# Kernel tuning notes

Measured on AMD Instinct MI355X. Metric: run time of the kernel, lower is better.

## Reference

```python
import jax, jax.numpy as jnp
import numpy as np

# --- hashgrid config (from __init__: num_levels=16, level_dim=4, base_res=2, log2_hashmap_size=19, desired_res=2048) ---
NUM_LEVELS = 16
LEVEL_DIM = 4
BASE_RES = 2
DESIRED_RES = 2048
TABLE_SIZE = 2 ** 19
_b = np.exp((np.log(DESIRED_RES) - np.log(BASE_RES)) / (NUM_LEVELS - 1))
SCALES = BASE_RES * _b ** np.arange(NUM_LEVELS) - 1.0          # instant-ngp per-level scale
RES = (np.ceil(SCALES) + 1).astype(np.int64)                   # per-level grid resolution
PRIME = np.uint32(2654435761)                                  # 2D spatial hash prime


def softplus10(x):
    return jax.nn.softplus(10.0 * x) / 10.0


def hash_encode(u, tables):
    """u: [P,2] in [0,1]; tables: [L, TABLE_SIZE, LEVEL_DIM]. Returns [P, L*LEVEL_DIM]."""
    outs = []
    for l in range(NUM_LEVELS):
        s = float(SCALES[l])
        res = int(RES[l])
        pos = u * s + 0.5
        pf = jnp.floor(pos)
        fr = pos - pf                      # bilinear fractions, [P,2]
        pi = pf.astype(jnp.int32)
        acc = None
        for dx in (0, 1):
            for dy in (0, 1):
                cx = pi[:, 0] + dx
                cy = pi[:, 1] + dy
                if res * res <= TABLE_SIZE:
                    idx = cy * res + cx                                   # dense level
                else:
                    idx = (cx.astype(jnp.uint32) ^ (cy.astype(jnp.uint32) * PRIME)) % jnp.uint32(TABLE_SIZE)
                    idx = idx.astype(jnp.int32)                           # hashed level
                wx = fr[:, 0] if dx else 1.0 - fr[:, 0]
                wy = fr[:, 1] if dy else 1.0 - fr[:, 1]
                term = tables[l][idx] * (wx * wy)[:, None]                # gather + bilerp
                acc = term if acc is None else acc + term
        outs.append(acc)
    return jnp.concatenate(outs, axis=-1)


def setup_inputs() -> dict:
    key = jax.random.key(0)
    ks = jax.random.split(key, 4)
    B, N, T = 4, 2048, 192
    x = jax.random.normal(ks[0], (B, N, T, 2), jnp.float32)
    embeddings = jax.random.normal(ks[1], (NUM_LEVELS, TABLE_SIZE, LEVEL_DIM), jnp.float32) * 1e-2
    W0 = jax.random.normal(ks[2], (64, 64), jnp.float32) / 8.0
    b0 = jnp.zeros((64,), jnp.float32)
    W1 = jax.random.normal(ks[3], (64, 1), jnp.float32) / 8.0
    b1 = jnp.zeros((1,), jnp.float32)
    return {"x": x, "embeddings": embeddings, "W0": W0, "b0": b0, "W1": W1, "b1": b1}


def reference(x, embeddings, W0, b0, W1, b1):
    B, N, T = x.shape[:3]
    xf = x.reshape(-1, T, 2)                       # [B*N, T, 2]
    rays_o = xf[:, 0]
    rd = xf[:, -1] - xf[:, 0]
    rd = rd / jnp.linalg.norm(rd, axis=-1, keepdims=True)
    z = jnp.linspace(0.0, 2.0, T)                  # [T]
    sample_dist = 1.0 / T
    xys = rays_o[:, None, :] + rd[:, None, :] * z[None, :, None]   # [B*N, T, 2]
    xys = jnp.clip(xys, -1.0, 1.0)                 # aabb clamp [-1,-1,1,1]
    u = (xys.reshape(-1, 2) + 1.0) * 0.5           # map [-bound,bound] -> [0,1], bound=1
    feats = hash_encode(u, embeddings)             # [P, 64]
    h = softplus10(feats @ W0 + b0)
    sigma = softplus10(h @ W1 + b1).reshape(-1, T) # [B*N, T]
    deltas = jnp.concatenate([jnp.full((1,), sample_dist, sigma.dtype), z[1:] - z[:-1]])  # [T]
    density = (deltas[None, :] * sigma).reshape(B, N, T)
    return density
```

## Files before the change

kernel.cpp:

```cpp
#include <hip/hip_runtime.h>
#include <cmath>

#define NUM_LEVELS 16
#define TABLE_SIZE 524288
#define TMASK (TABLE_SIZE - 1)
#define HASH_PRIME 2654435761u
#define T_SAMPLES 192
#define BLOCK 256
#define PTS 64

typedef __bf16 bf16x8 __attribute__((ext_vector_type(8)));
typedef __bf16 bf16x4 __attribute__((ext_vector_type(4)));
typedef float f32x4 __attribute__((ext_vector_type(4)));

struct LvlParams {
    float s[NUM_LEVELS];
    int   res[NUM_LEVELS];
    int   hashed[NUM_LEVELS];
};

__device__ __forceinline__ float softplus10(float x) {
    float t = 10.0f * x;
    float e = __expf(-fabsf(t));
    return (fmaxf(t, 0.0f) + __logf(1.0f + e)) * 0.1f;
}

typedef __attribute__((address_space(1))) const void CGV;
typedef __attribute__((address_space(3))) void LDSV;

__device__ __forceinline__ void dma_gather16(const void* gaddr, void* lds_wave_base) {
    __builtin_amdgcn_global_load_lds((CGV*)gaddr, (LDSV*)lds_wave_base, 16, 0, 0);
}

__device__ __forceinline__ void corner_idx(int cx, int cy, int res, int hashed,
                                           int& i00, int& i01, int& i10, int& i11) {
    if (hashed) {
        unsigned hy0 = (unsigned)cy * HASH_PRIME;
        unsigned hy1 = (unsigned)(cy + 1) * HASH_PRIME;
        i00 = (int)(((unsigned)cx ^ hy0) & TMASK);
        i01 = (int)(((unsigned)cx ^ hy1) & TMASK);
        i10 = (int)(((unsigned)(cx + 1) ^ hy0) & TMASK);
        i11 = (int)(((unsigned)(cx + 1) ^ hy1) & TMASK);
    } else {
        i00 = cy * res + cx; i10 = i00 + 1;
        i01 = i00 + res;     i11 = i01 + 1;
    }
}

__device__ __forceinline__ bf16x4 lerp4(f32x4 c00, f32x4 c01, f32x4 c10, f32x4 c11,
                                        float fx, float fy) {
    float w00 = (1.0f - fx) * (1.0f - fy), w01 = (1.0f - fx) * fy;
    float w10 = fx * (1.0f - fy),          w11 = fx * fy;
    f32x4 a = c00 * w00 + c01 * w01 + c10 * w10 + c11 * w11;
    bf16x4 r;
    r[0] = (__bf16)a.x; r[1] = (__bf16)a.y; r[2] = (__bf16)a.z; r[3] = (__bf16)a.w;
    return r;
}

__global__ void prep(const float* __restrict__ W0, __bf16* __restrict__ w0f,
                     float* __restrict__ sArr, int* __restrict__ resArr,
                     int* __restrict__ hashArr, LvlParams lp) {
    const int t = threadIdx.x;
    if (t < NUM_LEVELS) {
        sArr[t] = lp.s[t]; resArr[t] = lp.res[t]; hashArr[t] = lp.hashed[t];
    }
    #pragma unroll
    for (int i = 0; i < 16; ++i) {
        int f = t * 16 + i;
        int j = f & 7, lx = (f >> 3) & 15, q = (f >> 7) & 3, nt = (f >> 9) & 3, kc = f >> 11;
        int k = kc * 32 + q * 8 + j;
        int n = nt * 16 + lx;
        w0f[f] = (__bf16)W0[k * 64 + n];
    }
}

__launch_bounds__(BLOCK, 5)
__global__ void nerf_fused(const float* __restrict__ x,
                           const float* __restrict__ emb,
                           const __bf16* __restrict__ w0f,
                           const float* __restrict__ sArr,
                           const int* __restrict__ resArr,
                           const int* __restrict__ hashArr,
                           const float* __restrict__ b0,
                           const float* __restrict__ W1,
                           const float* __restrict__ b1,
                           float* __restrict__ out) {
    __shared__ __align__(16) f32x4 land[16 * 64];
    __shared__ __align__(16) __bf16 feS[PTS][72];

    const int tid  = threadIdx.x;
    const int lane = tid & 63, w = tid >> 6;

    const int gp  = blockIdx.x * PTS + lane;
    const int ray = gp / T_SAMPLES;
    const int t   = gp - ray * T_SAMPLES;

    const float2 o  = *(const float2*)(x + (size_t)ray * (T_SAMPLES * 2));
    const float2 ep = *(const float2*)(x + (size_t)ray * (T_SAMPLES * 2) + (T_SAMPLES - 1) * 2);
    float rdx = ep.x - o.x, rdy = ep.y - o.y;
    float inv = 1.0f / sqrtf(rdx * rdx + rdy * rdy);
    rdx *= inv; rdy *= inv;
    const float z = (float)((double)t * (2.0 / 191.0));
    float px = fminf(fmaxf(o.x + rdx * z, -1.0f), 1.0f);
    float py = fminf(fmaxf(o.y + rdy * z, -1.0f), 1.0f);
    const float ux = (px + 1.0f) * 0.5f;
    const float uy = (py + 1.0f) * 0.5f;

    const int l0 = w, l1 = w + 4, l2 = w + 8, l3 = w + 12;

    float fx3, fy3;
    {
        float s = sArr[l3];
        float posx = ux * s + 0.5f, posy = uy * s + 0.5f;
        float pfx = floorf(posx), pfy = floorf(posy);
        fx3 = posx - pfx; fy3 = posy - pfy;
        int cx = (int)pfx, cy = (int)pfy;
        int i00, i01, i10, i11;
        corner_idx(cx, cy, resArr[l3], hashArr[l3], i00, i01, i10, i11);
        const f32x4* tb = (const f32x4*)(emb + (size_t)l3 * (TABLE_SIZE * 4));
        dma_gather16(tb + i00, land + (w * 4 + 0) * 64);
        dma_gather16(tb + i01, land + (w * 4 + 1) * 64);
        dma_gather16(tb + i10, land + (w * 4 + 2) * 64);
        dma_gather16(tb + i11, land + (w * 4 + 3) * 64);
    }

    f32x4 cre[4]; float fx2, fy2;
    {
        float s = sArr[l2];
        float posx = ux * s + 0.5f, posy = uy * s + 0.5f;
        float pfx = floorf(posx), pfy = floorf(posy);
        fx2 = posx - pfx; fy2 = posy - pfy;
        int cx = (int)pfx, cy = (int)pfy;
        int res = resArr[l2];
        int i00 = cy * res + cx, i10 = i00 + 1, i01 = i00 + res, i11 = i01 + 1;
        const f32x4* tb = (const f32x4*)(emb + (size_t)l2 * (TABLE_SIZE * 4));
        cre[0] = tb[i00]; cre[1] = tb[i01]; cre[2] = tb[i10]; cre[3] = tb[i11];
    }

    f32x4 c1v[4]; float fx1, fy1;
    {
        float s = sArr[l1];
        float posx = ux * s + 0.5f, posy = uy * s + 0.5f;
        float pfx = floorf(posx), pfy = floorf(posy);
        fx1 = posx - pfx; fy1 = posy - pfy;
        int cx = (int)pfx, cy = (int)pfy;
        int res = resArr[l1];
        int i00 = cy * res + cx, i10 = i00 + 1, i01 = i00 + res, i11 = i01 + 1;
        const f32x4* tb = (const f32x4*)(emb + (size_t)l1 * (TABLE_SIZE * 4));
        c1v[0] = tb[i00]; c1v[1] = tb[i01]; c1v[2] = tb[i10]; c1v[3] = tb[i11];
    }
    f32x4 c0v[4]; float fx0, fy0;
    {
        float s = sArr[l0];
        float posx = ux * s + 0.5f, posy = uy * s + 0.5f;
        float pfx = floorf(posx), pfy = floorf(posy);
        fx0 = posx - pfx; fy0 = posy - pfy;
        int cx = (int)pfx, cy = (int)pfy;
        int res = resArr[l0];
        int i00 = cy * res + cx, i10 = i00 + 1, i01 = i00 + res, i11 = i01 + 1;
        const f32x4* tb = (const f32x4*)(emb + (size_t)l0 * (TABLE_SIZE * 4));
        c0v[0] = tb[i00]; c0v[1] = tb[i01]; c0v[2] = tb[i10]; c0v[3] = tb[i11];
    }

    *(bf16x4*)&feS[lane][l0 * 4] = lerp4(c0v[0], c0v[1], c0v[2], c0v[3], fx0, fy0);
    *(bf16x4*)&feS[lane][l1 * 4] = lerp4(c1v[0], c1v[1], c1v[2], c1v[3], fx1, fy1);
    *(bf16x4*)&feS[lane][l2 * 4] = lerp4(cre[0], cre[1], cre[2], cre[3], fx2, fy2);

    __builtin_amdgcn_s_waitcnt(0x0F70);
    {
        f32x4 c00 = land[(w * 4 + 0) * 64 + lane];
        f32x4 c01 = land[(w * 4 + 1) * 64 + lane];
        f32x4 c10 = land[(w * 4 + 2) * 64 + lane];
        f32x4 c11 = land[(w * 4 + 3) * 64 + lane];
        *(bf16x4*)&feS[lane][l3 * 4] = lerp4(c00, c01, c10, c11, fx3, fy3);
    }

    __syncthreads();

    const int lx = lane & 15, q = lane >> 4;

    f32x4 acc[4];
    #pragma unroll
    for (int nt = 0; nt < 4; ++nt) acc[nt] = (f32x4)(0.0f);

    #pragma unroll
    for (int kc = 0; kc < 2; ++kc) {
        bf16x8 afr = *(const bf16x8*)&feS[w * 16 + lx][kc * 32 + q * 8];
        #pragma unroll
        for (int nt = 0; nt < 4; ++nt) {
            bf16x8 bfr = *(const bf16x8*)(w0f + (size_t)(((kc * 4 + nt) * 4 + q) * 16 + lx) * 8);
            acc[nt] = __builtin_amdgcn_mfma_f32_16x16x32_bf16(afr, bfr, acc[nt], 0, 0, 0);
        }
    }

    float b0v[4], w1v[4];
    #pragma unroll
    for (int nt = 0; nt < 4; ++nt) {
        b0v[nt] = b0[nt * 16 + lx];
        w1v[nt] = W1[nt * 16 + lx];
    }
    const float b1v = b1[0];
    const float d0 = (float)(1.0 / 192.0);
    const float d1 = (float)(2.0 / 191.0);

    float part[4];
    #pragma unroll
    for (int r = 0; r < 4; ++r) {
        float p = 0.0f;
        #pragma unroll
        for (int nt = 0; nt < 4; ++nt)
            p += softplus10(acc[nt][r] + b0v[nt]) * w1v[nt];
        p += __shfl_xor(p, 1, 64);
        p += __shfl_xor(p, 2, 64);
        p += __shfl_xor(p, 4, 64);
        p += __shfl_xor(p, 8, 64);
        part[r] = p;
    }
    if (lx == 0) {
        const int g0 = blockIdx.x * PTS + w * 16 + q * 4;
        const int tt = g0 % T_SAMPLES;
        f32x4 ov;
        ov.x = softplus10(part[0] + b1v) * (tt == 0 ? d0 : d1);
        ov.y = softplus10(part[1] + b1v) * d1;
        ov.z = softplus10(part[2] + b1v) * d1;
        ov.w = softplus10(part[3] + b1v) * d1;
        *(f32x4*)(out + g0) = ov;
    }
}

extern "C" void kernel_launch(void* const* d_in, const int* in_sizes, int n_in,
                              void* d_out, int out_size, void* d_ws, size_t ws_size,
                              hipStream_t stream) {
    const float* x   = (const float*)d_in[0];
    const float* emb = (const float*)d_in[1];
    const float* W0  = (const float*)d_in[2];
    const float* b0  = (const float*)d_in[3];
    const float* W1  = (const float*)d_in[4];
    const float* b1  = (const float*)d_in[5];
    float* out = (float*)d_out;

    char* ws = (char*)d_ws;
    __bf16* w0f   = (__bf16*)ws;
    float* sArr   = (float*)(ws + 8192);
    int*   resArr = (int*)(ws + 8256);
    int*   hashArr= (int*)(ws + 8320);

    LvlParams lp;
    const double bb = std::exp((std::log(2048.0) - std::log(2.0)) / 15.0);
    for (int l = 0; l < NUM_LEVELS; ++l) {
        double sc = 2.0 * std::pow(bb, (double)l) - 1.0;
        int rr = (int)std::ceil(sc) + 1;
        lp.s[l] = (float)sc;
        lp.res[l] = rr;
        lp.hashed[l] = ((long long)rr * (long long)rr > (long long)TABLE_SIZE) ? 1 : 0;
    }

    prep<<<1, 256, 0, stream>>>(W0, w0f, sArr, resArr, hashArr, lp);

    const int nblk = out_size / PTS;
    nerf_fused<<<nblk, BLOCK, 0, stream>>>(x, emb, w0f, sArr, resArr, hashArr,
                                           b0, W1, b1, out);
}
```

Baseline: 371.3 us.

## Replace LDS DMA gather with register loads, level-major feature LDS layout

```diff
diff --git a/kernel.cpp b/kernel.cpp
--- a/kernel.cpp
+++ b/kernel.cpp
@@ -23,13 +23,6 @@
     float t = 10.0f * x;
     float e = __expf(-fabsf(t));
     return (fmaxf(t, 0.0f) + __logf(1.0f + e)) * 0.1f;
-}
-
-typedef __attribute__((address_space(1))) const void CGV;
-typedef __attribute__((address_space(3))) void LDSV;
-
-__device__ __forceinline__ void dma_gather16(const void* gaddr, void* lds_wave_base) {
-    __builtin_amdgcn_global_load_lds((CGV*)gaddr, (LDSV*)lds_wave_base, 16, 0, 0);
 }
 
 __device__ __forceinline__ void corner_idx(int cx, int cy, int res, int hashed,
@@ -74,7 +67,7 @@
     }
 }
 
-__launch_bounds__(BLOCK, 5)
+__launch_bounds__(BLOCK, 8)
 __global__ void nerf_fused(const float* __restrict__ x,
                            const float* __restrict__ emb,
                            const __bf16* __restrict__ w0f,
@@ -85,8 +78,7 @@
                            const float* __restrict__ W1,
                            const float* __restrict__ b1,
                            float* __restrict__ out) {
-    __shared__ __align__(16) f32x4 land[16 * 64];
-    __shared__ __align__(16) __bf16 feS[PTS][72];
+    __shared__ __align__(16) __bf16 feT[NUM_LEVELS * PTS * 4];
 
     const int tid  = threadIdx.x;
     const int lane = tid & 63, w = tid >> 6;
@@ -108,7 +100,7 @@
 
     const int l0 = w, l1 = w + 4, l2 = w + 8, l3 = w + 12;
 
-    float fx3, fy3;
+    f32x4 c3v[4]; float fx3, fy3;
     {
         float s = sArr[l3];
         float posx = ux * s + 0.5f, posy = uy * s + 0.5f;
@@ -118,66 +110,54 @@
         int i00, i01, i10, i11;
         corner_idx(cx, cy, resArr[l3], hashArr[l3], i00, i01, i10, i11);
         const f32x4* tb = (const f32x4*)(emb + (size_t)l3 * (TABLE_SIZE * 4));
-        dma_gather16(tb + i00, land + (w * 4 + 0) * 64);
-        dma_gather16(tb + i01, land + (w * 4 + 1) * 64);
-        dma_gather16(tb + i10, land + (w * 4 + 2) * 64);
-        dma_gather16(tb + i11, land + (w * 4 + 3) * 64);
-    }
-
-    f32x4 cre[4]; float fx2, fy2;
+        c3v[0] = tb[i00]; c3v[1] = tb[i01]; c3v[2] = tb[i10]; c3v[3] = tb[i11];
+    }
+
     {
         float s = sArr[l2];
         float posx = ux * s + 0.5f, posy = uy * s + 0.5f;
         float pfx = floorf(posx), pfy = floorf(posy);
-        fx2 = posx - pfx; fy2 = posy - pfy;
+        float fx = posx - pfx, fy = posy - pfy;
         int cx = (int)pfx, cy = (int)pfy;
         int res = resArr[l2];
         int i00 = cy * res + cx, i10 = i00 + 1, i01 = i00 + res, i11 = i01 + 1;
         const f32x4* tb = (const f32x4*)(emb + (size_t)l2 * (TABLE_SIZE * 4));
-        cre[0] = tb[i00]; cre[1] = tb[i01]; cre[2] = tb[i10]; cre[3] = tb[i11];
-    }
-
-    f32x4 c1v[4]; float fx1, fy1;
+        f32x4 a = tb[i00], b = tb[i01], c = tb[i10], d = tb[i11];
+        *(bf16x4*)&feT[(l2 * PTS + lane) * 4] = lerp4(a, b, c, d, fx, fy);
+    }
+
     {
         float s = sArr[l1];
         float posx = ux * s + 0.5f, posy = uy * s + 0.5f;
         float pfx = floorf(posx), pfy = floorf(posy);
-        fx1 = posx - pfx; fy1 = posy - pfy;
+        float fx = posx - pfx, fy = posy - pfy;
         int cx = (int)pfx, cy = (int)pfy;
         int res = resArr[l1];
         int i00 = cy * res + cx, i10 = i00 + 1, i01 = i00 + res, i11 = i01 + 1;
         const f32x4* tb = (const f32x4*)(emb + (size_t)l1 * (TABLE_SIZE * 4));
-        c1v[0] = tb[i00]; c1v[1] = tb[i01]; c1v[2] = tb[i10]; c1v[3] = tb[i11];
-    }
-    f32x4 c0v[4]; float fx0, fy0;
+        f32x4 a = tb[i00], b = tb[i01], c = tb[i10], d = tb[i11];
+        *(bf16x4*)&feT[(l1 * PTS + lane) * 4] = lerp4(a, b, c, d, fx, fy);
+    }
+
     {
         float s = sArr[l0];
         float posx = ux * s + 0.5f, posy = uy * s + 0.5f;
         float pfx = floorf(posx), pfy = floorf(posy);
-        fx0 = posx - pfx; fy0 = posy - pfy;
+        float fx = posx - pfx, fy = posy - pfy;
         int cx = (int)pfx, cy = (int)pfy;
         int res = resArr[l0];
         int i00 = cy * res + cx, i10 = i00 + 1, i01 = i00 + res, i11 = i01 + 1;
         const f32x4* tb = (const f32x4*)(emb + (size_t)l0 * (TABLE_SIZE * 4));
-        c0v[0] = tb[i00]; c0v[1] = tb[i01]; c0v[2] = tb[i10]; c0v[3] = tb[i11];
-    }
-
-    *(bf16x4*)&feS[lane][l0 * 4] = lerp4(c0v[0], c0v[1], c0v[2], c0v[3], fx0, fy0);
-    *(bf16x4*)&feS[lane][l1 * 4] = lerp4(c1v[0], c1v[1], c1v[2], c1v[3], fx1, fy1);
-    *(bf16x4*)&feS[lane][l2 * 4] = lerp4(cre[0], cre[1], cre[2], cre[3], fx2, fy2);
-
-    __builtin_amdgcn_s_waitcnt(0x0F70);
-    {
-        f32x4 c00 = land[(w * 4 + 0) * 64 + lane];
-        f32x4 c01 = land[(w * 4 + 1) * 64 + lane];
-        f32x4 c10 = land[(w * 4 + 2) * 64 + lane];
-        f32x4 c11 = land[(w * 4 + 3) * 64 + lane];
-        *(bf16x4*)&feS[lane][l3 * 4] = lerp4(c00, c01, c10, c11, fx3, fy3);
-    }
+        f32x4 a = tb[i00], b = tb[i01], c = tb[i10], d = tb[i11];
+        *(bf16x4*)&feT[(l0 * PTS + lane) * 4] = lerp4(a, b, c, d, fx, fy);
+    }
+
+    *(bf16x4*)&feT[(l3 * PTS + lane) * 4] = lerp4(c3v[0], c3v[1], c3v[2], c3v[3], fx3, fy3);
 
     __syncthreads();
 
     const int lx = lane & 15, q = lane >> 4;
+    const int p  = w * 16 + lx;
 
     f32x4 acc[4];
     #pragma unroll
@@ -185,7 +165,10 @@
 
     #pragma unroll
     for (int kc = 0; kc < 2; ++kc) {
-        bf16x8 afr = *(const bf16x8*)&feS[w * 16 + lx][kc * 32 + q * 8];
+        const int la = kc * 8 + 2 * q;
+        bf16x4 lo = *(const bf16x4*)&feT[(la * PTS + p) * 4];
+        bf16x4 hi = *(const bf16x4*)&feT[((la + 1) * PTS + p) * 4];
+        bf16x8 afr = __builtin_shufflevector(lo, hi, 0, 1, 2, 3, 4, 5, 6, 7);
         #pragma unroll
         for (int nt = 0; nt < 4; ++nt) {
             bf16x8 bfr = *(const bf16x8*)(w0f + (size_t)(((kc * 4 + nt) * 4 + q) * 16 + lx) * 8);
@@ -206,15 +189,15 @@
     float part[4];
     #pragma unroll
     for (int r = 0; r < 4; ++r) {
-        float p = 0.0f;
+        float pp = 0.0f;
         #pragma unroll
         for (int nt = 0; nt < 4; ++nt)
-            p += softplus10(acc[nt][r] + b0v[nt]) * w1v[nt];
-        p += __shfl_xor(p, 1, 64);
-        p += __shfl_xor(p, 2, 64);
-        p += __shfl_xor(p, 4, 64);
-        p += __shfl_xor(p, 8, 64);
-        part[r] = p;
+            pp += softplus10(acc[nt][r] + b0v[nt]) * w1v[nt];
+        pp += __shfl_xor(pp, 1, 64);
+        pp += __shfl_xor(pp, 2, 64);
+        pp += __shfl_xor(pp, 4, 64);
+        pp += __shfl_xor(pp, 8, 64);
+        part[r] = pp;
     }
     if (lx == 0) {
         const int g0 = blockIdx.x * PTS + w * 16 + q * 4;
```

Result: no change. 378.7 us (+2.0%).
